# Kernel tuning notes

Hardware: AMD Instinct MI355X
Metric: run time of the kernel (lower is better)

The kernel has to match this reference:

```python
import jax, jax.numpy as jnp
import numpy as np

B, S, D, H = 4, 2048, 1024, 16
HD = D // H  # head_dim = 64

def setup_inputs() -> dict:
    key = jax.random.key(0)
    ks = jax.random.split(key, 6)
    scale = 1.0 / np.sqrt(D)
    x = jax.random.normal(ks[0], (B, S, D), dtype=jnp.float32)
    Wq = jax.random.normal(ks[1], (D, D), dtype=jnp.float32) * scale
    Wk = jax.random.normal(ks[2], (D, D), dtype=jnp.float32) * scale
    Wv = jax.random.normal(ks[3], (D, D), dtype=jnp.float32) * scale
    Wo = jax.random.normal(ks[4], (D, D), dtype=jnp.float32) * scale
    z = jnp.zeros((D,), dtype=jnp.float32)
    return {"x": x, "Wq": Wq, "bq": z, "Wk": Wk, "bk": z, "Wv": Wv, "bv": z, "Wo": Wo, "bo": z}

def reference(x, Wq, bq, Wk, bk, Wv, bv, Wo, bo):
    b, s, d = x.shape
    hd = d // H
    def split_heads(t):
        return t.reshape(b, s, H, hd).swapaxes(1, 2)  # [B,H,S,hd]
    q = split_heads(x @ Wq + bq)
    k = split_heads(x @ Wk + bk)
    v = split_heads(x @ Wv + bv)
    logits = jnp.einsum('bhqd,bhkd->bhqk', q, k) / jnp.sqrt(jnp.asarray(hd, x.dtype))
    attn = jax.nn.softmax(logits, axis=-1)
    vals = jnp.einsum('bhqk,bhkd->bhqd', attn, v)
    vals = vals.swapaxes(1, 2).reshape(b, s, d)
    return vals @ Wo + bo
```

## Files before the change

kernel.cpp:

```cpp
#include <hip/hip_runtime.h>
#include <hip/hip_bf16.h>
#include <cstdint>
#include <cstddef>


typedef __attribute__((ext_vector_type(8))) short short8;
typedef __attribute__((ext_vector_type(8))) unsigned short ushort8;
typedef __attribute__((ext_vector_type(4))) unsigned short ushort4v;
typedef __attribute__((ext_vector_type(4))) float floatx4;

#define LOG2E 1.44269504088896340736f
#define QSCALE (0.125f * LOG2E)

__device__ __forceinline__ unsigned short f2bf(float f) {
  union { float f; unsigned int u; } c; c.f = f;
  return (unsigned short)((c.u + 0x7fffu + ((c.u >> 16) & 1u)) >> 16);
}

__device__ __forceinline__ unsigned int pack_bf16(float a, float b) {
  unsigned int ua = __builtin_bit_cast(unsigned int, a) + 0x8000u;
  unsigned int ub = __builtin_bit_cast(unsigned int, b) + 0x8000u;
  return __builtin_amdgcn_perm(ub, ua, 0x07060302);
}

__device__ __forceinline__ float fexp2(float x) {
#if __HIP_DEVICE_COMPILE__
  return __builtin_amdgcn_exp2f(x);
#else
  return x;
#endif
}

__device__ __forceinline__ void gl_lds16(const void* g, void* l) {
  __builtin_amdgcn_global_load_lds((__attribute__((address_space(1))) void*)g,
                                   (__attribute__((address_space(3))) void*)l, 16, 0, 0);
}

__global__ __launch_bounds__(256) void cast_x_kernel(const float* __restrict__ x,
                                                     unsigned short* __restrict__ xb, int n4) {
  int i = blockIdx.x * 256 + threadIdx.x;
  if (i >= n4) return;
  float4 v = ((const float4*)x)[i];
  ushort4v o;
  o.x = f2bf(v.x); o.y = f2bf(v.y); o.z = f2bf(v.z); o.w = f2bf(v.w);
  ((ushort4v*)xb)[i] = o;
}

__global__ __launch_bounds__(256) void transpose_w_kernel(
    const float* __restrict__ Wq, const float* __restrict__ Wk,
    const float* __restrict__ Wv, const float* __restrict__ Wo,
    unsigned short* __restrict__ Wqkv_t, unsigned short* __restrict__ Wo_t) {
  __shared__ float tile[32][33];
  const int which = blockIdx.z;
  const float* src = (which == 0) ? Wq : (which == 1) ? Wk : (which == 2) ? Wv : Wo;
  unsigned short* dst = (which == 3) ? Wo_t : (Wqkv_t + (size_t)which * 1024 * 1024);
  const int bn = blockIdx.x * 32;
  const int bk = blockIdx.y * 32;
  const int tx = threadIdx.x & 31, ty = threadIdx.x >> 5;
#pragma unroll
  for (int r = 0; r < 32; r += 8)
    tile[ty + r][tx] = src[(size_t)(bk + ty + r) * 1024 + bn + tx];
  __syncthreads();
#pragma unroll
  for (int r = 0; r < 32; r += 8)
    dst[(size_t)(bn + ty + r) * 1024 + bk + tx] = f2bf(tile[tx][ty + r]);
}

template <int MODE>
__global__ __launch_bounds__(256, 3) void gemm_bt(
    const unsigned short* __restrict__ A, const unsigned short* __restrict__ Bt,
    int M, int N, int K,
    const float* __restrict__ bias0, const float* __restrict__ bias1,
    const float* __restrict__ bias2,
    unsigned short* __restrict__ outQ, unsigned short* __restrict__ outK,
    unsigned short* __restrict__ outVt, float* __restrict__ outF) {
  __shared__ unsigned short As[128 * 32];
  __shared__ unsigned short Bs[128 * 32];

  const int tid = threadIdx.x;
  const int lane = tid & 63;
  const int wid = tid >> 6;
  const int wm = wid >> 1, wn = wid & 1;
  const int l15 = lane & 15, q4 = lane >> 4;
  const int bm = blockIdx.x * 128, bn = blockIdx.y * 128;

  const int rowL = lane >> 2;
  const int segL = (lane & 3) * 16;

  const char* Ab = (const char*)A;
  const char* Bb = (const char*)Bt;
  const size_t strideA = (size_t)K * 2;

  floatx4 acc[4][4] = {};

  for (int k0 = 0; k0 < K; k0 += 32) {
    __syncthreads();
#pragma unroll
    for (int c0 = 0; c0 < 2; ++c0) {
      const int c = wid * 2 + c0;
      gl_lds16(Ab + (size_t)(bm + c * 16 + rowL) * strideA + (size_t)k0 * 2 + segL,
               &As[c * 512]);
      gl_lds16(Bb + (size_t)(bn + c * 16 + rowL) * strideA + (size_t)k0 * 2 + segL,
               &Bs[c * 512]);
    }
    __syncthreads();

    short8 af[4], bfr[4];
#pragma unroll
    for (int i = 0; i < 4; ++i)
      af[i] = *(const short8*)&As[(wm * 64 + i * 16 + l15) * 32 + q4 * 8];
#pragma unroll
    for (int j = 0; j < 4; ++j)
      bfr[j] = *(const short8*)&Bs[(wn * 64 + j * 16 + l15) * 32 + q4 * 8];
#pragma unroll
    for (int i = 0; i < 4; ++i)
#pragma unroll
      for (int j = 0; j < 4; ++j)
        acc[i][j] = __builtin_amdgcn_mfma_f32_16x16x32_bf16(af[i], bfr[j], acc[i][j], 0, 0, 0);
  }

  if (MODE == 0) {
    __syncthreads();
    unsigned short* scr = ((wid < 2) ? As : Bs) + (wid & 1) * 2048;
    const int region = bn >> 10;
    const float* bias = (region == 0) ? bias0 : (region == 1) ? bias1 : bias2;
    const int row0b = bm + wm * 64;
    const int b = row0b >> 11;
    const int colbase = (bn + wn * 64) & 1023;
    const int h = colbase >> 6;
    const size_t bh = (size_t)(b * 16 + h);
#pragma unroll
    for (int i = 0; i < 4; ++i) {
      const int s0 = (row0b + i * 16) & 2047;
#pragma unroll
      for (int j = 0; j < 4; ++j) {
        const int col = j * 16 + l15;
        const float bb = bias[colbase + col];
#pragma unroll
        for (int r = 0; r < 4; ++r) {
          float v = acc[i][j][r] + bb;
          if (region == 0) v *= QSCALE;
          scr[(q4 * 4 + r) * 66 + col] = f2bf(v);
        }
      }
      if (region <= 1) {
        unsigned short* dst = (region == 0) ? outQ : outK;
        ushort8 v0 = *(ushort8*)&scr[l15 * 66 + q4 * 16];
        ushort8 v1 = *(ushort8*)&scr[l15 * 66 + q4 * 16 + 8];
        unsigned short* orow = dst + (bh * 2048 + s0 + l15) * 64 + q4 * 16;
        *(ushort8*)orow = v0;
        *(ushort8*)(orow + 8) = v1;
      } else {
        const int hd = lane;
        unsigned short tmp[16];
#pragma unroll
        for (int r = 0; r < 16; ++r) tmp[r] = scr[r * 66 + hd];
        ushort8 v0, v1;
#pragma unroll
        for (int r = 0; r < 8; ++r) { v0[r] = tmp[r]; v1[r] = tmp[8 + r]; }
        unsigned short* orow = outVt + (bh * 64 + hd) * 2048 + s0;
        *(ushort8*)orow = v0;
        *(ushort8*)(orow + 8) = v1;
      }
      __syncthreads();
    }
  } else {
#pragma unroll
    for (int i = 0; i < 4; ++i) {
      const int row0 = bm + wm * 64 + i * 16 + q4 * 4;
#pragma unroll
      for (int j = 0; j < 4; ++j) {
        const int gn = bn + wn * 64 + j * 16 + l15;
        const float bb = bias0[gn];
#pragma unroll
        for (int r = 0; r < 4; ++r)
          outF[(size_t)(row0 + r) * N + gn] = acc[i][j][r] + bb;
      }
    }
  }
}

__global__ __launch_bounds__(256, 2) void flash_attn(
    const unsigned short* __restrict__ Q, const unsigned short* __restrict__ Kg,
    const unsigned short* __restrict__ Vt, unsigned short* __restrict__ Oout) {
  __shared__ unsigned short Ks[2][64 * 72];
  __shared__ unsigned short Vs[2][64 * 72];

  const int tid = threadIdx.x, lane = tid & 63, wid = tid >> 6;
  const int l15 = lane & 15, q4 = lane >> 4;
  const int bh = blockIdx.y;
  const int bb = bh >> 4, hh = bh & 15;
  const int q0 = blockIdx.x * 256;
  const size_t base = (size_t)bh * 2048 * 64;

  short8 qf[4][2];
#pragma unroll
  for (int s = 0; s < 4; ++s) {
    const unsigned short* qrow = Q + base + (size_t)(q0 + s * 64 + wid * 16 + l15) * 64;
    qf[s][0] = *(const short8*)(qrow + q4 * 8);
    qf[s][1] = *(const short8*)(qrow + 32 + q4 * 8);
  }

  const int sr = tid >> 2;
  const int sg = (tid & 3) * 16;
  const int loc = sr & 31;
  const int ph = (loc >> 4) & 1, pq = (loc >> 2) & 3, pr = loc & 3;
  const int gp = (sr & 32) + pq * 8 + ph * 4 + pr;
  const unsigned short* Kbase = Kg + base + (size_t)gp * 64 + sg;
  const unsigned short* Vbase = Vt + base + (size_t)sr * 2048 + sg;

  ushort8 kr0, kr1, vr0, vr1;
  kr0 = *(const ushort8*)Kbase;       kr1 = *(const ushort8*)(Kbase + 8);
  vr0 = *(const ushort8*)Vbase;       vr1 = *(const ushort8*)(Vbase + 8);
  *(ushort8*)&Ks[0][sr * 72 + sg] = kr0;  *(ushort8*)&Ks[0][sr * 72 + sg + 8] = kr1;
  *(ushort8*)&Vs[0][sr * 72 + sg] = vr0;  *(ushort8*)&Vs[0][sr * 72 + sg + 8] = vr1;
  kr0 = *(const ushort8*)(Kbase + 4096);  kr1 = *(const ushort8*)(Kbase + 4104);
  vr0 = *(const ushort8*)(Vbase + 64);    vr1 = *(const ushort8*)(Vbase + 72);

  floatx4 oacc[4][4] = {};
  float lsum[4] = {0.f, 0.f, 0.f, 0.f};

  for (int it = 0; it < 32; ++it) {
    const int cur = it & 1;
    __syncthreads();
    if (it < 31) {
      *(ushort8*)&Ks[cur ^ 1][sr * 72 + sg] = kr0;
      *(ushort8*)&Ks[cur ^ 1][sr * 72 + sg + 8] = kr1;
      *(ushort8*)&Vs[cur ^ 1][sr * 72 + sg] = vr0;
      *(ushort8*)&Vs[cur ^ 1][sr * 72 + sg + 8] = vr1;
    }
    if (it < 30) {
      const unsigned short* kp = Kbase + (size_t)(it + 2) * 4096;
      const unsigned short* vp = Vbase + (size_t)(it + 2) * 64;
      kr0 = *(const ushort8*)kp;       kr1 = *(const ushort8*)(kp + 8);
      vr0 = *(const ushort8*)vp;       vr1 = *(const ushort8*)(vp + 8);
    }

    short8 pf[4][2];
#pragma unroll
    for (int c = 0; c < 2; ++c) {
      floatx4 sc[4][2] = {};
#pragma unroll
      for (int tt = 0; tt < 2; ++tt) {
        const int t = 2 * c + tt;
        const unsigned short* krow = &Ks[cur][(t * 16 + l15) * 72];
        short8 kf0 = *(const short8*)(krow + q4 * 8);
        short8 kf1 = *(const short8*)(krow + 32 + q4 * 8);
#pragma unroll
        for (int s = 0; s < 4; ++s) {
          sc[s][tt] = __builtin_amdgcn_mfma_f32_16x16x32_bf16(kf0, qf[s][0], sc[s][tt], 0, 0, 0);
          sc[s][tt] = __builtin_amdgcn_mfma_f32_16x16x32_bf16(kf1, qf[s][1], sc[s][tt], 0, 0, 0);
        }
      }
#pragma unroll
      for (int s = 0; s < 4; ++s) {
        float e0 = fexp2(sc[s][0][0]), e1 = fexp2(sc[s][0][1]);
        float e2 = fexp2(sc[s][0][2]), e3 = fexp2(sc[s][0][3]);
        float e4 = fexp2(sc[s][1][0]), e5 = fexp2(sc[s][1][1]);
        float e6 = fexp2(sc[s][1][2]), e7 = fexp2(sc[s][1][3]);
        lsum[s] += ((e0 + e1) + (e2 + e3)) + ((e4 + e5) + (e6 + e7));
        union { unsigned int u[4]; short8 v; } cv;
        cv.u[0] = pack_bf16(e0, e1); cv.u[1] = pack_bf16(e2, e3);
        cv.u[2] = pack_bf16(e4, e5); cv.u[3] = pack_bf16(e6, e7);
        pf[s][c] = cv.v;
      }
    }

#pragma unroll
    for (int t = 0; t < 4; ++t) {
      const unsigned short* vrow = &Vs[cur][(t * 16 + l15) * 72 + q4 * 8];
      short8 vf0 = *(const short8*)vrow;
      short8 vf1 = *(const short8*)(vrow + 32);
#pragma unroll
      for (int s = 0; s < 4; ++s) {
        oacc[s][t] = __builtin_amdgcn_mfma_f32_16x16x32_bf16(vf0, pf[s][0], oacc[s][t], 0, 0, 0);
        oacc[s][t] = __builtin_amdgcn_mfma_f32_16x16x32_bf16(vf1, pf[s][1], oacc[s][t], 0, 0, 0);
      }
    }
  }

#pragma unroll
  for (int s = 0; s < 4; ++s) {
    float l = lsum[s];
    l += __shfl_xor(l, 16);
    l += __shfl_xor(l, 32);
    const float inv = 1.0f / l;
    const int srow = q0 + s * 64 + wid * 16 + l15;
    unsigned short* orow = Oout + ((size_t)bb * 2048 + srow) * 1024 + hh * 64;
#pragma unroll
    for (int t = 0; t < 4; ++t) {
      union { unsigned int u[2]; ushort4v s4; } cv;
      cv.u[0] = pack_bf16(oacc[s][t][0] * inv, oacc[s][t][1] * inv);
      cv.u[1] = pack_bf16(oacc[s][t][2] * inv, oacc[s][t][3] * inv);
      *(ushort4v*)(orow + t * 16 + q4 * 4) = cv.s4;
    }
  }
}

extern "C" void kernel_launch(void* const* d_in, const int* in_sizes, int n_in,
                              void* d_out, int out_size, void* d_ws, size_t ws_size,
                              hipStream_t stream) {
  const float* x  = (const float*)d_in[0];
  const float* Wq = (const float*)d_in[1];
  const float* bq = (const float*)d_in[2];
  const float* Wk = (const float*)d_in[3];
  const float* bk = (const float*)d_in[4];
  const float* Wv = (const float*)d_in[5];
  const float* bv = (const float*)d_in[6];
  const float* Wo = (const float*)d_in[7];
  const float* bo = (const float*)d_in[8];
  float* out = (float*)d_out;

  char* ws = (char*)d_ws;
  unsigned short* xb     = (unsigned short*)(ws);
  unsigned short* wqkv_t = (unsigned short*)(ws + (16u << 20));
  unsigned short* wo_t   = (unsigned short*)(ws + (22u << 20));
  unsigned short* Qb     = (unsigned short*)(ws + (24u << 20));
  unsigned short* Kb     = (unsigned short*)(ws + (40u << 20));
  unsigned short* Vtb    = (unsigned short*)(ws + (56u << 20));
  unsigned short* attn   = (unsigned short*)(ws + (72u << 20));
  (void)in_sizes; (void)n_in; (void)out_size; (void)ws_size;

  cast_x_kernel<<<dim3(8192), 256, 0, stream>>>(x, xb, 8192 * 1024 / 4);
  transpose_w_kernel<<<dim3(32, 32, 4), 256, 0, stream>>>(Wq, Wk, Wv, Wo, wqkv_t, wo_t);
  gemm_bt<0><<<dim3(64, 24), 256, 0, stream>>>(xb, wqkv_t, 8192, 3072, 1024,
                                               bq, bk, bv, Qb, Kb, Vtb, nullptr);
  flash_attn<<<dim3(8, 64), 256, 0, stream>>>(Qb, Kb, Vtb, attn);
  gemm_bt<1><<<dim3(64, 8), 256, 0, stream>>>(attn, wo_t, 8192, 1024, 1024,
                                              bo, nullptr, nullptr,
                                              nullptr, nullptr, nullptr, out);
}
```

Measured before the change: 276.8 us.

## Use direct global-to-LDS loads with XOR swizzle and smaller query tiles in attention

The flash attention kernel now stages K/V tiles through a direct global-to-LDS copy helper instead of register round-trips, and replaces the padded LDS layout with an XOR-swizzled unpadded one. Each block processes 128 queries instead of 256, which doubles the grid and raises the occupancy target to 4 blocks per CU. MFMA sections are wrapped in s_setprio to favour matrix issue. The aim is to cut register pressure and staging latency and to improve latency hiding, at the cost of loading each K/V tile twice as often across blocks.

```diff
diff --git a/kernel.cpp b/kernel.cpp
--- a/kernel.cpp
+++ b/kernel.cpp
@@ -180,80 +180,76 @@
   }
 }
 
-__global__ __launch_bounds__(256, 2) void flash_attn(
+__global__ __launch_bounds__(256, 4) void flash_attn(
     const unsigned short* __restrict__ Q, const unsigned short* __restrict__ Kg,
     const unsigned short* __restrict__ Vt, unsigned short* __restrict__ Oout) {
-  __shared__ unsigned short Ks[2][64 * 72];
-  __shared__ unsigned short Vs[2][64 * 72];
+  __shared__ __align__(128) unsigned short Ks[2][64 * 64];
+  __shared__ __align__(128) unsigned short Vs[2][64 * 64];
 
   const int tid = threadIdx.x, lane = tid & 63, wid = tid >> 6;
   const int l15 = lane & 15, q4 = lane >> 4;
   const int bh = blockIdx.y;
   const int bb = bh >> 4, hh = bh & 15;
-  const int q0 = blockIdx.x * 256;
+  const int q0 = blockIdx.x * 128;
   const size_t base = (size_t)bh * 2048 * 64;
 
-  short8 qf[4][2];
-#pragma unroll
-  for (int s = 0; s < 4; ++s) {
+  short8 qf[2][2];
+#pragma unroll
+  for (int s = 0; s < 2; ++s) {
     const unsigned short* qrow = Q + base + (size_t)(q0 + s * 64 + wid * 16 + l15) * 64;
     qf[s][0] = *(const short8*)(qrow + q4 * 8);
     qf[s][1] = *(const short8*)(qrow + 32 + q4 * 8);
   }
 
-  const int sr = tid >> 2;
-  const int sg = (tid & 3) * 16;
-  const int loc = sr & 31;
-  const int ph = (loc >> 4) & 1, pq = (loc >> 2) & 3, pr = loc & 3;
-  const int gp = (sr & 32) + pq * 8 + ph * 4 + pr;
-  const unsigned short* Kbase = Kg + base + (size_t)gp * 64 + sg;
-  const unsigned short* Vbase = Vt + base + (size_t)sr * 2048 + sg;
-
-  ushort8 kr0, kr1, vr0, vr1;
-  kr0 = *(const ushort8*)Kbase;       kr1 = *(const ushort8*)(Kbase + 8);
-  vr0 = *(const ushort8*)Vbase;       vr1 = *(const ushort8*)(Vbase + 8);
-  *(ushort8*)&Ks[0][sr * 72 + sg] = kr0;  *(ushort8*)&Ks[0][sr * 72 + sg + 8] = kr1;
-  *(ushort8*)&Vs[0][sr * 72 + sg] = vr0;  *(ushort8*)&Vs[0][sr * 72 + sg + 8] = vr1;
-  kr0 = *(const ushort8*)(Kbase + 4096);  kr1 = *(const ushort8*)(Kbase + 4104);
-  vr0 = *(const ushort8*)(Vbase + 64);    vr1 = *(const ushort8*)(Vbase + 72);
-
-  floatx4 oacc[4][4] = {};
-  float lsum[4] = {0.f, 0.f, 0.f, 0.f};
+  const int r0 = wid * 16 + (lane >> 3);
+  const int sg2 = ((lane & 7) ^ ((lane >> 3) & 7)) * 8;
+  auto gpf = [](int r) {
+    const int loc = r & 31;
+    return (r & 32) + ((loc >> 2) & 3) * 8 + ((loc >> 4) & 1) * 4 + (loc & 3);
+  };
+  const unsigned short* kp0 = Kg + base + (size_t)gpf(r0) * 64 + sg2;
+  const unsigned short* kp1 = Kg + base + (size_t)gpf(r0 + 8) * 64 + sg2;
+  const unsigned short* vp0 = Vt + base + (size_t)r0 * 2048 + sg2;
+  const unsigned short* vp1 = vp0 + 8 * 2048;
+
+  auto stage = [&](int b, int T) {
+    gl_lds16(kp0 + (size_t)T * 4096, &Ks[b][wid * 1024]);
+    gl_lds16(kp1 + (size_t)T * 4096, &Ks[b][wid * 1024 + 512]);
+    gl_lds16(vp0 + (size_t)T * 64,   &Vs[b][wid * 1024]);
+    gl_lds16(vp1 + (size_t)T * 64,   &Vs[b][wid * 1024 + 512]);
+  };
+
+  stage(0, 0);
+
+  floatx4 oacc[2][4] = {};
+  float lsum[2] = {0.f, 0.f};
+  const int fo0 = (q4 ^ (l15 & 7)) << 3;
 
   for (int it = 0; it < 32; ++it) {
     const int cur = it & 1;
     __syncthreads();
-    if (it < 31) {
-      *(ushort8*)&Ks[cur ^ 1][sr * 72 + sg] = kr0;
-      *(ushort8*)&Ks[cur ^ 1][sr * 72 + sg + 8] = kr1;
-      *(ushort8*)&Vs[cur ^ 1][sr * 72 + sg] = vr0;
-      *(ushort8*)&Vs[cur ^ 1][sr * 72 + sg + 8] = vr1;
-    }
-    if (it < 30) {
-      const unsigned short* kp = Kbase + (size_t)(it + 2) * 4096;
-      const unsigned short* vp = Vbase + (size_t)(it + 2) * 64;
-      kr0 = *(const ushort8*)kp;       kr1 = *(const ushort8*)(kp + 8);
-      vr0 = *(const ushort8*)vp;       vr1 = *(const ushort8*)(vp + 8);
-    }
-
-    short8 pf[4][2];
+    if (it < 31) stage(cur ^ 1, it + 1);
+
+    short8 pf[2][2];
 #pragma unroll
     for (int c = 0; c < 2; ++c) {
-      floatx4 sc[4][2] = {};
+      floatx4 sc[2][2] = {};
 #pragma unroll
       for (int tt = 0; tt < 2; ++tt) {
         const int t = 2 * c + tt;
-        const unsigned short* krow = &Ks[cur][(t * 16 + l15) * 72];
-        short8 kf0 = *(const short8*)(krow + q4 * 8);
-        short8 kf1 = *(const short8*)(krow + 32 + q4 * 8);
-#pragma unroll
-        for (int s = 0; s < 4; ++s) {
+        const unsigned short* krow = &Ks[cur][(t * 16 + l15) * 64];
+        short8 kf0 = *(const short8*)(krow + fo0);
+        short8 kf1 = *(const short8*)(krow + (fo0 ^ 32));
+        __builtin_amdgcn_s_setprio(1);
+#pragma unroll
+        for (int s = 0; s < 2; ++s) {
           sc[s][tt] = __builtin_amdgcn_mfma_f32_16x16x32_bf16(kf0, qf[s][0], sc[s][tt], 0, 0, 0);
           sc[s][tt] = __builtin_amdgcn_mfma_f32_16x16x32_bf16(kf1, qf[s][1], sc[s][tt], 0, 0, 0);
         }
-      }
-#pragma unroll
-      for (int s = 0; s < 4; ++s) {
+        __builtin_amdgcn_s_setprio(0);
+      }
+#pragma unroll
+      for (int s = 0; s < 2; ++s) {
         float e0 = fexp2(sc[s][0][0]), e1 = fexp2(sc[s][0][1]);
         float e2 = fexp2(sc[s][0][2]), e3 = fexp2(sc[s][0][3]);
         float e4 = fexp2(sc[s][1][0]), e5 = fexp2(sc[s][1][1]);
@@ -268,19 +264,21 @@
 
 #pragma unroll
     for (int t = 0; t < 4; ++t) {
-      const unsigned short* vrow = &Vs[cur][(t * 16 + l15) * 72 + q4 * 8];
-      short8 vf0 = *(const short8*)vrow;
-      short8 vf1 = *(const short8*)(vrow + 32);
-#pragma unroll
-      for (int s = 0; s < 4; ++s) {
+      const unsigned short* vrow = &Vs[cur][(t * 16 + l15) * 64];
+      short8 vf0 = *(const short8*)(vrow + fo0);
+      short8 vf1 = *(const short8*)(vrow + (fo0 ^ 32));
+      __builtin_amdgcn_s_setprio(1);
+#pragma unroll
+      for (int s = 0; s < 2; ++s) {
         oacc[s][t] = __builtin_amdgcn_mfma_f32_16x16x32_bf16(vf0, pf[s][0], oacc[s][t], 0, 0, 0);
         oacc[s][t] = __builtin_amdgcn_mfma_f32_16x16x32_bf16(vf1, pf[s][1], oacc[s][t], 0, 0, 0);
       }
-    }
-  }
-
-#pragma unroll
-  for (int s = 0; s < 4; ++s) {
+      __builtin_amdgcn_s_setprio(0);
+    }
+  }
+
+#pragma unroll
+  for (int s = 0; s < 2; ++s) {
     float l = lsum[s];
     l += __shfl_xor(l, 16);
     l += __shfl_xor(l, 32);
@@ -325,7 +323,7 @@
   transpose_w_kernel<<<dim3(32, 32, 4), 256, 0, stream>>>(Wq, Wk, Wv, Wo, wqkv_t, wo_t);
   gemm_bt<0><<<dim3(64, 24), 256, 0, stream>>>(xb, wqkv_t, 8192, 3072, 1024,
                                                bq, bk, bv, Qb, Kb, Vtb, nullptr);
-  flash_attn<<<dim3(8, 64), 256, 0, stream>>>(Qb, Kb, Vtb, attn);
+  flash_attn<<<dim3(16, 64), 256, 0, stream>>>(Qb, Kb, Vtb, attn);
   gemm_bt<1><<<dim3(64, 8), 256, 0, stream>>>(attn, wo_t, 8192, 1024, 1024,
                                               bo, nullptr, nullptr,
                                               nullptr, nullptr, nullptr, out);
```

Result: no change. 275.4 us (-0.5%).
